# Kernel optimization log

Measured on AMD Instinct MI355X. Metric: run time of the kernel, lower is better.

The kernel has to match this reference:

```python
import jax, jax.numpy as jnp
import numpy as np

D = 131072   # input_dim = 2*256*256
H = 512      # lstm_hidden_dim
OUT = 128    # out_dim


def _lstm_cell(x, h, c, W_ih, W_hh, b_ih, b_hh):
    # PyTorch LSTMCell: gates in order (i, f, g, o)
    gates = x @ W_ih.T + b_ih + h @ W_hh.T + b_hh  # [1, 4H]
    i, f, g, o = jnp.split(gates, 4, axis=-1)
    i = jax.nn.sigmoid(i)
    f = jax.nn.sigmoid(f)
    g = jnp.tanh(g)
    o = jax.nn.sigmoid(o)
    c_new = f * c + i * g
    h_new = o * jnp.tanh(c_new)
    return h_new, c_new


def setup_inputs() -> dict:
    key = jax.random.key(0)
    ks = jax.random.split(key, 20)
    s_ih = 1.0 / np.sqrt(H)
    inp = {
        "dL_dU": jax.random.normal(ks[0], (256, 256), jnp.float32),
        "dL_dV": jax.random.normal(ks[1], (256, 256), jnp.float32),
        "hidden": jax.random.normal(ks[2], (2, 1, H), jnp.float32),
        "cell": jax.random.normal(ks[3], (2, 1, H), jnp.float32),
        "W_ih1": jax.random.uniform(ks[4], (4 * H, D), jnp.float32, -s_ih, s_ih),
        "W_hh1": jax.random.uniform(ks[5], (4 * H, H), jnp.float32, -s_ih, s_ih),
        "b_ih1": jax.random.uniform(ks[6], (4 * H,), jnp.float32, -s_ih, s_ih),
        "b_hh1": jax.random.uniform(ks[7], (4 * H,), jnp.float32, -s_ih, s_ih),
        "W_ih2": jax.random.uniform(ks[8], (4 * H, H), jnp.float32, -s_ih, s_ih),
        "W_hh2": jax.random.uniform(ks[9], (4 * H, H), jnp.float32, -s_ih, s_ih),
        "b_ih2": jax.random.uniform(ks[10], (4 * H,), jnp.float32, -s_ih, s_ih),
        "b_hh2": jax.random.uniform(ks[11], (4 * H,), jnp.float32, -s_ih, s_ih),
        "W1": jax.random.uniform(ks[12], (OUT * OUT, H), jnp.float32, -s_ih, s_ih),
        "b1": jax.random.uniform(ks[13], (OUT * OUT,), jnp.float32, -s_ih, s_ih),
        "W2": jax.random.uniform(ks[14], (1, H), jnp.float32, -s_ih, s_ih),
        "b2": jax.random.uniform(ks[15], (1,), jnp.float32, -s_ih, s_ih),
        "W3": jax.random.uniform(ks[16], (1, H), jnp.float32, -s_ih, s_ih),
        "b3": jax.random.uniform(ks[17], (1,), jnp.float32, -s_ih, s_ih),
    }
    return inp


def reference(dL_dU, dL_dV, hidden, cell,
              W_ih1, W_hh1, b_ih1, b_hh1,
              W_ih2, W_hh2, b_ih2, b_hh2,
              W1, b1, W2, b2, W3, b3):
    grad_flat = jnp.concatenate([dL_dU.reshape(-1), dL_dV.reshape(-1)], axis=0)[None, :]  # [1, D]
    h0, c0 = _lstm_cell(grad_flat, hidden[0], cell[0], W_ih1, W_hh1, b_ih1, b_hh1)
    h1, c1 = _lstm_cell(h0, hidden[1], cell[1], W_ih2, W_hh2, b_ih2, b_hh2)
    g = (h1 @ W1.T + b1).reshape(OUT, OUT)
    step_size = jnp.clip(h1 @ W2.T + b2, 1e-07, 0.005)
    m_c = jnp.clip(2.0 * jnp.clip(h0 @ W3.T + b3, 0.0, 1.0), 0.0, 1.0)
    return (g, step_size, m_c, jnp.stack((h0, h1)), jnp.stack((c0, c1)))
```

## Files before the change

### kernel.cpp

```cpp
#include <hip/hip_runtime.h>
#include <math.h>

#define D_IN 131072
#define H 512
#define G4 2048
#define OUTN 16384

#define OFF_STEP 16384
#define OFF_MC   16385
#define OFF_H0   16386
#define OFF_H1   16898
#define OFF_C0   17410
#define OFF_C1   17922

__device__ __forceinline__ float sigmoidf_(float x) {
    return 1.0f / (1.0f + __expf(-x));
}

__device__ __forceinline__ float dot4(float4 a, float4 b) {
    return a.x*b.x + a.y*b.y + a.z*b.z + a.w*b.w;
}

typedef float f4v __attribute__((ext_vector_type(4)));
__device__ __forceinline__ float4 ntload4(const float4* p) {
    f4v v = __builtin_nontemporal_load((const f4v*)p);
    float4 r; r.x = v.x; r.y = v.y; r.z = v.z; r.w = v.w;
    return r;
}

__global__ __launch_bounds__(256) void k_gemv1p(
    const float* __restrict__ U, const float* __restrict__ V,
    const float* __restrict__ Wih, const float* __restrict__ Whh,
    const float* __restrict__ bih, const float* __restrict__ bhh,
    const float* __restrict__ hidden, float* __restrict__ gates)
{
    __shared__ float s[4];
    const int t = threadIdx.x;
    const float4* __restrict__ U4 = (const float4*)U;
    const float4* __restrict__ V4 = (const float4*)V;
    const float4* __restrict__ h4 = (const float4*)hidden;
    #pragma unroll 1
    for (int i = 0; i < 4; ++i) {
        const int r = blockIdx.x * 4 + i;
        const float4* __restrict__ Wrow = (const float4*)(Wih + (size_t)r * D_IN);
        float acc = 0.0f;
        #pragma unroll 4
        for (int idx = t; idx < 16384; idx += 256) {
            acc += dot4(ntload4(&Wrow[idx]), U4[idx]);
        }
        #pragma unroll 4
        for (int idx = t; idx < 16384; idx += 256) {
            acc += dot4(ntload4(&Wrow[idx + 16384]), V4[idx]);
        }
        if (t < 128) {
            const float4* __restrict__ Wh4 = (const float4*)(Whh + (size_t)r * H);
            acc += dot4(ntload4(&Wh4[t]), h4[t]);
        }
        #pragma unroll
        for (int off = 32; off > 0; off >>= 1) acc += __shfl_down(acc, off);
        if ((t & 63) == 0) s[t >> 6] = acc;
        __syncthreads();
        if (t == 0) {
            gates[r] = s[0] + s[1] + s[2] + s[3] + bih[r] + bhh[r];
        }
        __syncthreads();
    }
}

__global__ __launch_bounds__(1024) void k_l2fused(
    const float* __restrict__ gates1, const float* __restrict__ cell_in,
    const float* __restrict__ hidden,
    const float* __restrict__ Wih2, const float* __restrict__ Whh2,
    const float* __restrict__ bih2, const float* __restrict__ bhh2,
    const float* __restrict__ W3, const float* __restrict__ b3,
    float* __restrict__ gates2, float* __restrict__ out)
{
    __shared__ float h0s[H];
    __shared__ float red[16];
    const int tid = threadIdx.x;
    if (tid < H) {
        float ig = sigmoidf_(gates1[tid]);
        float fg = sigmoidf_(gates1[H + tid]);
        float gg = tanhf(gates1[2*H + tid]);
        float og = sigmoidf_(gates1[3*H + tid]);
        float c  = fg * cell_in[tid] + ig * gg;
        float h  = og * tanhf(c);
        h0s[tid] = h;
        if (blockIdx.x == 0) {
            out[OFF_H0 + tid] = h;
            out[OFF_C0 + tid] = c;
        }
    }
    __syncthreads();
    const int wv = tid >> 6, lane = tid & 63;
    const int row = blockIdx.x * 16 + wv;
    const float4* __restrict__ Wr = (const float4*)(Wih2 + (size_t)row * H);
    const float4* __restrict__ Hr = (const float4*)(Whh2 + (size_t)row * H);
    const float4* h4 = (const float4*)h0s;
    const float4* __restrict__ y4 = (const float4*)(hidden + H);
    float acc = dot4(ntload4(&Wr[lane]),      h4[lane])
              + dot4(ntload4(&Hr[lane]),      y4[lane])
              + dot4(ntload4(&Wr[lane + 64]), h4[lane + 64])
              + dot4(ntload4(&Hr[lane + 64]), y4[lane + 64]);
    #pragma unroll
    for (int off = 32; off > 0; off >>= 1) acc += __shfl_down(acc, off);
    if (lane == 0) gates2[row] = acc + bih2[row] + bhh2[row];

    if (blockIdx.x == 0) {
        float p = (tid < H) ? h0s[tid] * W3[tid] : 0.0f;
        #pragma unroll
        for (int off = 32; off > 0; off >>= 1) p += __shfl_down(p, off);
        if (lane == 0) red[wv] = p;
        __syncthreads();
        if (tid == 0) {
            float v = b3[0];
            #pragma unroll
            for (int i = 0; i < 16; ++i) v += red[i];
            v = fminf(fmaxf(v, 0.0f), 1.0f);
            out[OFF_MC] = fminf(2.0f * v, 1.0f);
        }
    }
}

__global__ __launch_bounds__(1024) void k_l3fused(
    const float* __restrict__ gates2, const float* __restrict__ cell_in,
    const float* __restrict__ W1, const float* __restrict__ b1,
    const float* __restrict__ W2, const float* __restrict__ b2,
    float* __restrict__ out)
{
    __shared__ float h1s[H];
    __shared__ float red[16];
    const int tid = threadIdx.x;
    if (tid < H) {
        float ig = sigmoidf_(gates2[tid]);
        float fg = sigmoidf_(gates2[H + tid]);
        float gg = tanhf(gates2[2*H + tid]);
        float og = sigmoidf_(gates2[3*H + tid]);
        float c  = fg * cell_in[H + tid] + ig * gg;
        float h  = og * tanhf(c);
        h1s[tid] = h;
        if (blockIdx.x == 0) {
            out[OFF_H1 + tid] = h;
            out[OFF_C1 + tid] = c;
        }
    }
    __syncthreads();
    const int wv = tid >> 6, lane = tid & 63;
    const int row = blockIdx.x * 16 + wv;
    const float4* __restrict__ Wr = (const float4*)(W1 + (size_t)row * H);
    const float4* h4 = (const float4*)h1s;
    float acc = dot4(ntload4(&Wr[lane]),      h4[lane])
              + dot4(ntload4(&Wr[lane + 64]), h4[lane + 64]);
    #pragma unroll
    for (int off = 32; off > 0; off >>= 1) acc += __shfl_down(acc, off);
    if (lane == 0) out[row] = acc + b1[row];

    if (blockIdx.x == 0) {
        float p = (tid < H) ? h1s[tid] * W2[tid] : 0.0f;
        #pragma unroll
        for (int off = 32; off > 0; off >>= 1) p += __shfl_down(p, off);
        if (lane == 0) red[wv] = p;
        __syncthreads();
        if (tid == 0) {
            float v = b2[0];
            #pragma unroll
            for (int i = 0; i < 16; ++i) v += red[i];
            out[OFF_STEP] = fminf(fmaxf(v, 1e-7f), 0.005f);
        }
    }
}

extern "C" void kernel_launch(void* const* d_in, const int* in_sizes, int n_in,
                              void* d_out, int out_size, void* d_ws, size_t ws_size,
                              hipStream_t stream) {
    const float* dL_dU  = (const float*)d_in[0];
    const float* dL_dV  = (const float*)d_in[1];
    const float* hidden = (const float*)d_in[2];
    const float* cell   = (const float*)d_in[3];
    const float* W_ih1  = (const float*)d_in[4];
    const float* W_hh1  = (const float*)d_in[5];
    const float* b_ih1  = (const float*)d_in[6];
    const float* b_hh1  = (const float*)d_in[7];
    const float* W_ih2  = (const float*)d_in[8];
    const float* W_hh2  = (const float*)d_in[9];
    const float* b_ih2  = (const float*)d_in[10];
    const float* b_hh2  = (const float*)d_in[11];
    const float* W1     = (const float*)d_in[12];
    const float* b1     = (const float*)d_in[13];
    const float* W2     = (const float*)d_in[14];
    const float* b2     = (const float*)d_in[15];
    const float* W3     = (const float*)d_in[16];
    const float* b3     = (const float*)d_in[17];

    float* out = (float*)d_out;
    float* ws  = (float*)d_ws;
    float* gates1 = ws;
    float* gates2 = ws + 2048;

    k_gemv1p<<<512, 256, 0, stream>>>(dL_dU, dL_dV, W_ih1, W_hh1,
                                      b_ih1, b_hh1, hidden, gates1);
    k_l2fused<<<G4 / 16, 1024, 0, stream>>>(gates1, cell, hidden,
                                            W_ih2, W_hh2, b_ih2, b_hh2,
                                            W3, b3, gates2, out);
    k_l3fused<<<OUTN / 16, 1024, 0, stream>>>(gates2, cell, W1, b1, W2, b2, out);
    (void)in_sizes; (void)n_in; (void)out_size; (void)ws_size;
}
```

Before: 188.0 us.

## Fuse three LSTM kernels into one cooperative kernel with grid syncs

Replaces the three separate kernel launches (layer-1 GEMV, layer-2 cell+GEMV, output projection) with a single cooperative kernel of 512 blocks of 256 threads that uses grid.sync between stages. The aim is to remove the launch gaps and tail effects between the three dependent stages. The later stages are remapped to 256-thread blocks, so the output projection now has each wave handle 8 rows. Grid-wide barriers add their own synchronisation cost, and stages 2 and 3 now run with fewer threads per block.

After: 313.2 us. +66.6%, slower.

```diff
diff --git a/kernel.cpp b/kernel.cpp
--- a/kernel.cpp
+++ b/kernel.cpp
@@ -1,5 +1,8 @@
 #include <hip/hip_runtime.h>
+#include <hip/hip_cooperative_groups.h>
 #include <math.h>
+
+namespace cg = cooperative_groups;
 
 #define D_IN 131072
 #define H 512
@@ -28,144 +31,144 @@
     return r;
 }
 
-__global__ __launch_bounds__(256) void k_gemv1p(
+__global__ __launch_bounds__(256) void k_fused(
     const float* __restrict__ U, const float* __restrict__ V,
-    const float* __restrict__ Wih, const float* __restrict__ Whh,
-    const float* __restrict__ bih, const float* __restrict__ bhh,
-    const float* __restrict__ hidden, float* __restrict__ gates)
+    const float* __restrict__ hidden, const float* __restrict__ cell,
+    const float* __restrict__ Wih1, const float* __restrict__ Whh1,
+    const float* __restrict__ bih1, const float* __restrict__ bhh1,
+    const float* __restrict__ Wih2, const float* __restrict__ Whh2,
+    const float* __restrict__ bih2, const float* __restrict__ bhh2,
+    const float* __restrict__ W1,   const float* __restrict__ b1,
+    const float* __restrict__ W2,   const float* __restrict__ b2,
+    const float* __restrict__ W3,   const float* __restrict__ b3,
+    float* __restrict__ gates1, float* __restrict__ gates2,
+    float* __restrict__ out)
 {
-    __shared__ float s[4];
+    cg::grid_group grid = cg::this_grid();
+    __shared__ float hs[H];
+    __shared__ float red[4];
     const int t = threadIdx.x;
-    const float4* __restrict__ U4 = (const float4*)U;
-    const float4* __restrict__ V4 = (const float4*)V;
-    const float4* __restrict__ h4 = (const float4*)hidden;
-    #pragma unroll 1
-    for (int i = 0; i < 4; ++i) {
-        const int r = blockIdx.x * 4 + i;
-        const float4* __restrict__ Wrow = (const float4*)(Wih + (size_t)r * D_IN);
-        float acc = 0.0f;
-        #pragma unroll 4
-        for (int idx = t; idx < 16384; idx += 256) {
-            acc += dot4(ntload4(&Wrow[idx]), U4[idx]);
-        }
-        #pragma unroll 4
-        for (int idx = t; idx < 16384; idx += 256) {
-            acc += dot4(ntload4(&Wrow[idx + 16384]), V4[idx]);
-        }
-        if (t < 128) {
-            const float4* __restrict__ Wh4 = (const float4*)(Whh + (size_t)r * H);
-            acc += dot4(ntload4(&Wh4[t]), h4[t]);
-        }
+    const int wv = t >> 6, lane = t & 63;
+
+    {
+        const float4* __restrict__ U4 = (const float4*)U;
+        const float4* __restrict__ V4 = (const float4*)V;
+        const float4* __restrict__ h4 = (const float4*)hidden;
+        #pragma unroll 1
+        for (int i = 0; i < 4; ++i) {
+            const int r = blockIdx.x * 4 + i;
+            const float4* __restrict__ Wrow = (const float4*)(Wih1 + (size_t)r * D_IN);
+            float acc = 0.0f;
+            #pragma unroll 4
+            for (int idx = t; idx < 16384; idx += 256) {
+                acc += dot4(ntload4(&Wrow[idx]), U4[idx]);
+            }
+            #pragma unroll 4
+            for (int idx = t; idx < 16384; idx += 256) {
+                acc += dot4(ntload4(&Wrow[idx + 16384]), V4[idx]);
+            }
+            if (t < 128) {
+                const float4* __restrict__ Wh4 = (const float4*)(Whh1 + (size_t)r * H);
+                acc += dot4(ntload4(&Wh4[t]), h4[t]);
+            }
+            #pragma unroll
+            for (int off = 32; off > 0; off >>= 1) acc += __shfl_down(acc, off);
+            if ((t & 63) == 0) red[t >> 6] = acc;
+            __syncthreads();
+            if (t == 0) {
+                gates1[r] = red[0] + red[1] + red[2] + red[3] + bih1[r] + bhh1[r];
+            }
+            __syncthreads();
+        }
+    }
+    grid.sync();
+
+    {
+        #pragma unroll
+        for (int k = 0; k < 2; ++k) {
+            const int j = t + k * 256;
+            float ig = sigmoidf_(gates1[j]);
+            float fg = sigmoidf_(gates1[H + j]);
+            float gg = tanhf(gates1[2*H + j]);
+            float og = sigmoidf_(gates1[3*H + j]);
+            float c  = fg * cell[j] + ig * gg;
+            float h  = og * tanhf(c);
+            hs[j] = h;
+            if (blockIdx.x == 0) {
+                out[OFF_H0 + j] = h;
+                out[OFF_C0 + j] = c;
+            }
+        }
+        __syncthreads();
+        const int row = blockIdx.x * 4 + wv;
+        const float4* __restrict__ Wr = (const float4*)(Wih2 + (size_t)row * H);
+        const float4* __restrict__ Hr = (const float4*)(Whh2 + (size_t)row * H);
+        const float4* h4 = (const float4*)hs;
+        const float4* __restrict__ y4 = (const float4*)(hidden + H);
+        float acc = dot4(ntload4(&Wr[lane]),      h4[lane])
+                  + dot4(ntload4(&Hr[lane]),      y4[lane])
+                  + dot4(ntload4(&Wr[lane + 64]), h4[lane + 64])
+                  + dot4(ntload4(&Hr[lane + 64]), y4[lane + 64]);
         #pragma unroll
         for (int off = 32; off > 0; off >>= 1) acc += __shfl_down(acc, off);
-        if ((t & 63) == 0) s[t >> 6] = acc;
+        if (lane == 0) gates2[row] = acc + bih2[row] + bhh2[row];
+
+        if (blockIdx.x == 0) {
+            float p = hs[t] * W3[t] + hs[t + 256] * W3[t + 256];
+            #pragma unroll
+            for (int off = 32; off > 0; off >>= 1) p += __shfl_down(p, off);
+            __syncthreads();
+            if (lane == 0) red[wv] = p;
+            __syncthreads();
+            if (t == 0) {
+                float v = red[0] + red[1] + red[2] + red[3] + b3[0];
+                v = fminf(fmaxf(v, 0.0f), 1.0f);
+                out[OFF_MC] = fminf(2.0f * v, 1.0f);
+            }
+        }
+    }
+    grid.sync();
+
+    {
         __syncthreads();
-        if (t == 0) {
-            gates[r] = s[0] + s[1] + s[2] + s[3] + bih[r] + bhh[r];
+        #pragma unroll
+        for (int k = 0; k < 2; ++k) {
+            const int j = t + k * 256;
+            float ig = sigmoidf_(gates2[j]);
+            float fg = sigmoidf_(gates2[H + j]);
+            float gg = tanhf(gates2[2*H + j]);
+            float og = sigmoidf_(gates2[3*H + j]);
+            float c  = fg * cell[H + j] + ig * gg;
+            float h  = og * tanhf(c);
+            hs[j] = h;
+            if (blockIdx.x == 0) {
+                out[OFF_H1 + j] = h;
+                out[OFF_C1 + j] = c;
+            }
         }
         __syncthreads();
-    }
-}
-
-__global__ __launch_bounds__(1024) void k_l2fused(
-    const float* __restrict__ gates1, const float* __restrict__ cell_in,
-    const float* __restrict__ hidden,
-    const float* __restrict__ Wih2, const float* __restrict__ Whh2,
-    const float* __restrict__ bih2, const float* __restrict__ bhh2,
-    const float* __restrict__ W3, const float* __restrict__ b3,
-    float* __restrict__ gates2, float* __restrict__ out)
-{
-    __shared__ float h0s[H];
-    __shared__ float red[16];
-    const int tid = threadIdx.x;
-    if (tid < H) {
-        float ig = sigmoidf_(gates1[tid]);
-        float fg = sigmoidf_(gates1[H + tid]);
-        float gg = tanhf(gates1[2*H + tid]);
-        float og = sigmoidf_(gates1[3*H + tid]);
-        float c  = fg * cell_in[tid] + ig * gg;
-        float h  = og * tanhf(c);
-        h0s[tid] = h;
+        const float4* h4 = (const float4*)hs;
+        #pragma unroll 2
+        for (int k = 0; k < 8; ++k) {
+            const int row = blockIdx.x * 32 + wv * 8 + k;
+            const float4* __restrict__ Wr = (const float4*)(W1 + (size_t)row * H);
+            float acc = dot4(ntload4(&Wr[lane]),      h4[lane])
+                      + dot4(ntload4(&Wr[lane + 64]), h4[lane + 64]);
+            #pragma unroll
+            for (int off = 32; off > 0; off >>= 1) acc += __shfl_down(acc, off);
+            if (lane == 0) out[row] = acc + b1[row];
+        }
         if (blockIdx.x == 0) {
-            out[OFF_H0 + tid] = h;
-            out[OFF_C0 + tid] = c;
-        }
-    }
-    __syncthreads();
-    const int wv = tid >> 6, lane = tid & 63;
-    const int row = blockIdx.x * 16 + wv;
-    const float4* __restrict__ Wr = (const float4*)(Wih2 + (size_t)row * H);
-    const float4* __restrict__ Hr = (const float4*)(Whh2 + (size_t)row * H);
-    const float4* h4 = (const float4*)h0s;
-    const float4* __restrict__ y4 = (const float4*)(hidden + H);
-    float acc = dot4(ntload4(&Wr[lane]),      h4[lane])
-              + dot4(ntload4(&Hr[lane]),      y4[lane])
-              + dot4(ntload4(&Wr[lane + 64]), h4[lane + 64])
-              + dot4(ntload4(&Hr[lane + 64]), y4[lane + 64]);
-    #pragma unroll
-    for (int off = 32; off > 0; off >>= 1) acc += __shfl_down(acc, off);
-    if (lane == 0) gates2[row] = acc + bih2[row] + bhh2[row];
-
-    if (blockIdx.x == 0) {
-        float p = (tid < H) ? h0s[tid] * W3[tid] : 0.0f;
-        #pragma unroll
-        for (int off = 32; off > 0; off >>= 1) p += __shfl_down(p, off);
-        if (lane == 0) red[wv] = p;
-        __syncthreads();
-        if (tid == 0) {
-            float v = b3[0];
-            #pragma unroll
-            for (int i = 0; i < 16; ++i) v += red[i];
-            v = fminf(fmaxf(v, 0.0f), 1.0f);
-            out[OFF_MC] = fminf(2.0f * v, 1.0f);
-        }
-    }
-}
-
-__global__ __launch_bounds__(1024) void k_l3fused(
-    const float* __restrict__ gates2, const float* __restrict__ cell_in,
-    const float* __restrict__ W1, const float* __restrict__ b1,
-    const float* __restrict__ W2, const float* __restrict__ b2,
-    float* __restrict__ out)
-{
-    __shared__ float h1s[H];
-    __shared__ float red[16];
-    const int tid = threadIdx.x;
-    if (tid < H) {
-        float ig = sigmoidf_(gates2[tid]);
-        float fg = sigmoidf_(gates2[H + tid]);
-        float gg = tanhf(gates2[2*H + tid]);
-        float og = sigmoidf_(gates2[3*H + tid]);
-        float c  = fg * cell_in[H + tid] + ig * gg;
-        float h  = og * tanhf(c);
-        h1s[tid] = h;
-        if (blockIdx.x == 0) {
-            out[OFF_H1 + tid] = h;
-            out[OFF_C1 + tid] = c;
-        }
-    }
-    __syncthreads();
-    const int wv = tid >> 6, lane = tid & 63;
-    const int row = blockIdx.x * 16 + wv;
-    const float4* __restrict__ Wr = (const float4*)(W1 + (size_t)row * H);
-    const float4* h4 = (const float4*)h1s;
-    float acc = dot4(ntload4(&Wr[lane]),      h4[lane])
-              + dot4(ntload4(&Wr[lane + 64]), h4[lane + 64]);
-    #pragma unroll
-    for (int off = 32; off > 0; off >>= 1) acc += __shfl_down(acc, off);
-    if (lane == 0) out[row] = acc + b1[row];
-
-    if (blockIdx.x == 0) {
-        float p = (tid < H) ? h1s[tid] * W2[tid] : 0.0f;
-        #pragma unroll
-        for (int off = 32; off > 0; off >>= 1) p += __shfl_down(p, off);
-        if (lane == 0) red[wv] = p;
-        __syncthreads();
-        if (tid == 0) {
-            float v = b2[0];
-            #pragma unroll
-            for (int i = 0; i < 16; ++i) v += red[i];
-            out[OFF_STEP] = fminf(fmaxf(v, 1e-7f), 0.005f);
+            float p = hs[t] * W2[t] + hs[t + 256] * W2[t + 256];
+            #pragma unroll
+            for (int off = 32; off > 0; off >>= 1) p += __shfl_down(p, off);
+            __syncthreads();
+            if (lane == 0) red[wv] = p;
+            __syncthreads();
+            if (t == 0) {
+                float v = red[0] + red[1] + red[2] + red[3] + b2[0];
+                out[OFF_STEP] = fminf(fmaxf(v, 1e-7f), 0.005f);
+            }
         }
     }
 }
@@ -197,11 +200,15 @@
     float* gates1 = ws;
     float* gates2 = ws + 2048;
 
-    k_gemv1p<<<512, 256, 0, stream>>>(dL_dU, dL_dV, W_ih1, W_hh1,
-                                      b_ih1, b_hh1, hidden, gates1);
-    k_l2fused<<<G4 / 16, 1024, 0, stream>>>(gates1, cell, hidden,
-                                            W_ih2, W_hh2, b_ih2, b_hh2,
-                                            W3, b3, gates2, out);
-    k_l3fused<<<OUTN / 16, 1024, 0, stream>>>(gates2, cell, W1, b1, W2, b2, out);
+    void* args[] = {
+        (void*)&dL_dU, (void*)&dL_dV, (void*)&hidden, (void*)&cell,
+        (void*)&W_ih1, (void*)&W_hh1, (void*)&b_ih1, (void*)&b_hh1,
+        (void*)&W_ih2, (void*)&W_hh2, (void*)&b_ih2, (void*)&b_hh2,
+        (void*)&W1, (void*)&b1, (void*)&W2, (void*)&b2,
+        (void*)&W3, (void*)&b3,
+        (void*)&gates1, (void*)&gates2, (void*)&out
+    };
+    hipLaunchCooperativeKernel((const void*)k_fused, dim3(512), dim3(256),
+                               args, 0, stream);
     (void)in_sizes; (void)n_in; (void)out_size; (void)ws_size;
 }
```
